# Kernel tuning notes

Hardware: AMD Instinct MI355X
Metric: run time of the kernel (lower is better)

The kernel has to match this reference:

```python
import jax, jax.numpy as jnp
import numpy as np

B, N, D = 512, 128, 768
TAU = 1.0            # NeuralSort temperature (allRank default)
COS_W = 0.1          # cosine_loss_weight
EPS = 1e-10          # allRank DEFAULT_EPS
PAD = -1.0           # allRank PADDED_Y_VALUE
SINKHORN_ITERS = 50
SINKHORN_TOL = 1e-6


def setup_inputs() -> dict:
    key = jax.random.key(0)
    kq, kr, ky = jax.random.split(key, 3)
    return {
        "query_embeddings": jax.random.normal(kq, (B, N, D), jnp.float32),
        "response_embeddings": jax.random.normal(kr, (B, N, D), jnp.float32),
        "labels": jax.random.uniform(ky, (B, N), dtype=jnp.float32),
    }


def _cosine_similarity(a, b):
    # torch.cosine_similarity semantics: clamp each norm at 1e-8
    num = jnp.sum(a * b, axis=-1)
    den = jnp.maximum(jnp.linalg.norm(a, axis=-1), 1e-8) * jnp.maximum(jnp.linalg.norm(b, axis=-1), 1e-8)
    return num / den


def _deterministic_neural_sort(s, tau, mask):
    # s: [B, N, 1] scores; mask: [B, N] padding mask (True = padded)
    n = s.shape[1]
    s = jnp.where(mask[:, :, None], -1e8, s)
    A = jnp.abs(s - jnp.swapaxes(s, 1, 2))                       # [B,N,N]
    pair_or = mask[:, :, None] | mask[:, None, :]
    A = jnp.where(pair_or, 0.0, A)
    Bmat = jnp.sum(A, axis=2, keepdims=True)                     # == A @ (1 1^T), broadcasts over cols
    valid = n - jnp.sum(mask, axis=1)                            # [B] number of non-padded items
    idx = jnp.arange(n)
    # per-row scaling vector: (n-m) - 1 - 2*j for j < n-m, else 0
    scaling = jnp.where(idx[None, :] < valid[:, None],
                        (valid[:, None] - 1 - 2 * idx[None, :]).astype(s.dtype), 0.0)
    s0 = jnp.where(mask[:, :, None], 0.0, s)
    C = s0 * scaling[:, None, :]                                 # [B,N,N] = s @ scaling^T
    P_max = jnp.swapaxes(C - Bmat, 1, 2)
    P_max = jnp.where(pair_or, -jnp.inf, P_max)
    P_max = jnp.where(mask[:, :, None] & mask[:, None, :], 1.0, P_max)
    return jax.nn.softmax(P_max / tau, axis=-1)


def _sinkhorn(mat, mask):
    pair_or = mask[:, None, :] | mask[:, :, None]
    pair_and = mask[:, None, :] & mask[:, :, None]
    mat = jnp.where(pair_or, 0.0, mat)
    mat = jnp.where(pair_and, 1.0, mat)

    def step(carry, _):
        m, done = carry
        m1 = m / jnp.maximum(jnp.sum(m, axis=1, keepdims=True), EPS)
        m2 = m1 / jnp.maximum(jnp.sum(m1, axis=2, keepdims=True), EPS)
        conv = (jnp.max(jnp.abs(jnp.sum(m2, axis=2) - 1.0)) < SINKHORN_TOL) & \
               (jnp.max(jnp.abs(jnp.sum(m2, axis=1) - 1.0)) < SINKHORN_TOL)
        new_m = jnp.where(done, m, m2)   # freeze once converged (emulates torch early break)
        return (new_m, done | conv), None

    (mat, _), _ = jax.lax.scan(step, (mat, jnp.array(False)), None, length=SINKHORN_ITERS)
    mat = jnp.where(pair_or, 0.0, mat)
    mat = jnp.where(pair_and, 1.0, mat)
    return mat


def _idcg_at_k(y_true, k):
    # allRank dcg(y_true, y_true, ats=[k]) with powered gains (no padding present)
    sorted_true = -jnp.sort(-y_true, axis=1)                     # descending
    gains = jnp.power(2.0, sorted_true) - 1.0
    discounts = 1.0 / jnp.log2(jnp.arange(y_true.shape[1], dtype=jnp.float32) + 2.0)
    return jnp.cumsum(gains * discounts, axis=1)[:, k - 1]       # [B]


def _forward(query_embeddings, response_embeddings, labels):
    scores = _cosine_similarity(query_embeddings, response_embeddings)   # [B,N]
    y_true = labels
    mask = (y_true == PAD)
    k = N                                                                # k=None -> slate length
    P_hat = _deterministic_neural_sort(scores[:, :, None], TAU, mask)    # [B,N,N]
    P_hat = _sinkhorn(P_hat, mask)
    P_hat = jnp.where(mask[:, :, None] | mask[:, None, :], 0.0, P_hat)
    g = jnp.power(2.0, jnp.where(mask, 0.0, y_true)) - 1.0               # powered relevancies
    ground_truth = jnp.einsum('bij,bj->bi', P_hat, g)                    # approx-sorted gains
    discounts = 1.0 / jnp.log2(jnp.arange(N, dtype=jnp.float32) + 2.0)
    discounted = ground_truth * discounts
    idcg = _idcg_at_k(y_true, k)                                         # [B]
    ndcg = jnp.sum(discounted[:, :k], axis=-1) / (idcg + EPS)
    idcg_zero = idcg == 0.0
    ndcg = jnp.where(idcg_zero, 0.0, ndcg)
    mean_ndcg = jnp.sum(ndcg) / jnp.maximum(jnp.sum(~idcg_zero), 1)
    ndcg_loss = 1.0 - mean_ndcg                                          # 1 + neuralNDCG = 1 - mean_ndcg
    cosine_loss = jnp.mean((scores - labels) ** 2)
    return (1.0 - COS_W) * ndcg_loss + COS_W * cosine_loss


def reference(query_embeddings, response_embeddings, labels):
    return _forward(query_embeddings, response_embeddings, labels)
```

## Files before the change

### kernel.cpp

```cpp
#include <hip/hip_runtime.h>
#include <math.h>

#define BB 512
#define NN 128
#define DD 768

__global__ __launch_bounds__(256, 2) void k_ndcg(const float* __restrict__ q,
                                                 const float* __restrict__ r,
                                                 const float* __restrict__ labels,
                                                 float* __restrict__ ndcg_out,
                                                 float* __restrict__ valid_out,
                                                 float* __restrict__ mse_out) {
    __shared__ float s_s[NN];
    __shared__ float s_B[NN];
    __shared__ float s_lab[NN];
    __shared__ float s_g[NN];
    __shared__ float s_u[NN];
    __shared__ float s_v[NN];
    __shared__ float s_rmax[NN];
    __shared__ float s_red[NN];
    __shared__ float s_mse[NN];
    __shared__ float s_gv[NN];
    __shared__ float s_wred[4];
    __shared__ float s_idcg[1];

    const int tid = threadIdx.x;
    const int b   = blockIdx.x;
    const int wv  = tid >> 6;
    const int ln  = tid & 63;
    const int p   = tid >> 1;
    const int h   = tid & 1;

    if (tid < NN) {
        float lv = labels[b * NN + tid];
        s_lab[tid] = lv;
        s_g[tid]   = exp2f(lv) - 1.0f;
    }

    const float4* q4 = (const float4*)(q + (size_t)b * NN * DD);
    const float4* r4 = (const float4*)(r + (size_t)b * NN * DD);
    for (int m = 0; m < 32; ++m) {
        const int row = wv + 4 * m;
        const float4* qa = q4 + row * (DD / 4);
        const float4* ra = r4 + row * (DD / 4);
        float qr = 0.f, qq = 0.f, rr2 = 0.f;
#pragma unroll
        for (int k = 0; k < 3; ++k) {
            float4 a = qa[ln + 64 * k];
            float4 c = ra[ln + 64 * k];
            qr  += a.x*c.x + a.y*c.y + a.z*c.z + a.w*c.w;
            qq  += a.x*a.x + a.y*a.y + a.z*a.z + a.w*a.w;
            rr2 += c.x*c.x + c.y*c.y + c.z*c.z + c.w*c.w;
        }
#pragma unroll
        for (int off = 32; off >= 1; off >>= 1) {
            qr  += __shfl_xor(qr, off);
            qq  += __shfl_xor(qq, off);
            rr2 += __shfl_xor(rr2, off);
        }
        if (ln == 0) {
            float den = fmaxf(sqrtf(qq), 1e-8f) * fmaxf(sqrtf(rr2), 1e-8f);
            s_s[row] = qr / den;
        }
    }
    __syncthreads();

    if (tid < NN) {
        float si = s_s[tid];
        float acc = 0.f;
        for (int j = 0; j < NN; ++j) acc += fabsf(si - s_s[j]);
        s_B[tid] = acc;
        float li = s_lab[tid];
        int rank = 0;
        for (int j = 0; j < NN; ++j) {
            float lj = s_lab[j];
            rank += (lj > li) || (lj == li && j < tid);
        }
        s_red[tid] = s_g[tid] / log2f((float)(rank + 2));
        float d = si - li;
        s_mse[tid] = d * d;
    }
    __syncthreads();
    if (tid < 32) {
        float v = s_red[tid] + s_red[tid + 32] + s_red[tid + 64] + s_red[tid + 96];
#pragma unroll
        for (int off = 16; off >= 1; off >>= 1) v += __shfl_xor(v, off);
        if (tid == 0) s_idcg[0] = v;
    } else if (tid < 64) {
        int t2 = tid - 32;
        float v = s_mse[t2] + s_mse[t2 + 32] + s_mse[t2 + 64] + s_mse[t2 + 96];
#pragma unroll
        for (int off = 16; off >= 1; off >>= 1) v = v + __shfl_xor(v, off);
        if (t2 == 0) mse_out[b] = v;
    }

    float u_p;
    float4 kr[16];
    {
        const float scal = (float)(127 - 2 * p);
        const float4* s4a = (const float4*)s_s;
        const float4* B4a = (const float4*)s_B;
        float rmax = -1e30f;
#pragma unroll
        for (int k = 0; k < 16; ++k) {
            float4 sv = s4a[16 * h + k];
            float4 Bv = B4a[16 * h + k];
            float4 v;
            v.x = sv.x * scal - Bv.x;
            v.y = sv.y * scal - Bv.y;
            v.z = sv.z * scal - Bv.z;
            v.w = sv.w * scal - Bv.w;
            kr[k] = v;
            rmax = fmaxf(rmax, fmaxf(fmaxf(v.x, v.y), fmaxf(v.z, v.w)));
        }
        rmax = fmaxf(rmax, __shfl_xor(rmax, 1));
        float rsum = 0.f;
#pragma unroll
        for (int k = 0; k < 16; ++k) {
            float4 v = kr[k];
            v.x = expf(v.x - rmax);
            v.y = expf(v.y - rmax);
            v.z = expf(v.z - rmax);
            v.w = expf(v.w - rmax);
            kr[k] = v;
            rsum += v.x + v.y + v.z + v.w;
        }
        rsum += __shfl_xor(rsum, 1);
        u_p = 1.0f / rsum;
        if (h == 0) { s_u[p] = u_p; s_rmax[p] = rmax; }
    }
    __syncthreads();

    float4 kc[16];
    {
        const float sp = s_s[p];
        const float Bp = s_B[p];
        const float4* rm4 = (const float4*)s_rmax;
#pragma unroll
        for (int k = 0; k < 16; ++k) {
            float4 rm = rm4[16 * h + k];
            const float base = (float)(127 - 2 * (64 * h + 4 * k));
            float4 e;
            e.x = expf(sp * base          - Bp - rm.x);
            e.y = expf(sp * (base - 2.f)  - Bp - rm.y);
            e.z = expf(sp * (base - 4.f)  - Bp - rm.z);
            e.w = expf(sp * (base - 6.f)  - Bp - rm.w);
            kc[k] = e;
        }
    }

    float v_p = 1.0f;
    const float4* u4 = (const float4*)s_u;
    const float4* v4 = (const float4*)s_v;
    for (int it = 0; it < 50; ++it) {
        float a = 0.f;
#pragma unroll
        for (int k = 0; k < 16; ++k) {
            float4 uu = u4[16 * h + k];
            float4 kk = kc[k];
            a += uu.x*kk.x + uu.y*kk.y + uu.z*kk.z + uu.w*kk.w;
        }
        a += __shfl_xor(a, 1);
        float cs  = v_p * a;
        float dev = fabsf(cs - 1.0f);
#pragma unroll
        for (int off = 2; off <= 32; off <<= 1) dev = fmaxf(dev, __shfl_xor(dev, off));
        if (ln == 0) s_wred[wv] = dev;
        __syncthreads();
        float devmax = fmaxf(fmaxf(s_wred[0], s_wred[1]), fmaxf(s_wred[2], s_wred[3]));
        if (it > 0 && devmax < 1e-6f) break;
        v_p = v_p / fmaxf(cs, 1e-10f);
        if (h == 0) s_v[p] = v_p;
        __syncthreads();
        float bb = 0.f;
#pragma unroll
        for (int k = 0; k < 16; ++k) {
            float4 vv = v4[16 * h + k];
            float4 kk = kr[k];
            bb += vv.x*kk.x + vv.y*kk.y + vv.z*kk.z + vv.w*kk.w;
        }
        bb += __shfl_xor(bb, 1);
        float rsm = u_p * bb;
        u_p = u_p / fmaxf(rsm, 1e-10f);
        if (h == 0) s_u[p] = u_p;
        __syncthreads();
    }

    if (tid < NN) s_gv[tid] = s_g[tid] * s_v[tid];
    __syncthreads();
    {
        const float4* gv4 = (const float4*)s_gv;
        float acc = 0.f;
#pragma unroll
        for (int k = 0; k < 16; ++k) {
            float4 gv = gv4[16 * h + k];
            float4 kk = kr[k];
            acc += kk.x*gv.x + kk.y*gv.y + kk.z*gv.z + kk.w*gv.w;
        }
        acc += __shfl_xor(acc, 1);
        if (h == 0) s_red[p] = u_p * acc / log2f((float)(p + 2));
    }
    __syncthreads();
    if (tid < 32) {
        float v = s_red[tid] + s_red[tid + 32] + s_red[tid + 64] + s_red[tid + 96];
#pragma unroll
        for (int off = 16; off >= 1; off >>= 1) v += __shfl_xor(v, off);
        if (tid == 0) {
            float idcg = s_idcg[0];
            bool zero = (idcg == 0.0f);
            ndcg_out[b]  = zero ? 0.0f : v / (idcg + 1e-10f);
            valid_out[b] = zero ? 0.0f : 1.0f;
        }
    }
}

__global__ __launch_bounds__(256) void k_final(const float* __restrict__ ndcg,
                                               const float* __restrict__ valid,
                                               const float* __restrict__ mse,
                                               float* __restrict__ out) {
    __shared__ float red[3][4];
    const int tid = threadIdx.x;
    const int lane = tid & 63, wv = tid >> 6;
    float nsum = ndcg[tid] + ndcg[tid + 256];
    float vsum = valid[tid] + valid[tid + 256];
    float msum = mse[tid] + mse[tid + 256];
#pragma unroll
    for (int off = 32; off >= 1; off >>= 1) {
        nsum += __shfl_xor(nsum, off);
        vsum += __shfl_xor(vsum, off);
        msum += __shfl_xor(msum, off);
    }
    if (lane == 0) { red[0][wv] = nsum; red[1][wv] = vsum; red[2][wv] = msum; }
    __syncthreads();
    if (tid == 0) {
        float n = red[0][0] + red[0][1] + red[0][2] + red[0][3];
        float v = red[1][0] + red[1][1] + red[1][2] + red[1][3];
        float m = red[2][0] + red[2][1] + red[2][2] + red[2][3];
        float mean_ndcg = n / fmaxf(v, 1.0f);
        out[0] = 0.9f * (1.0f - mean_ndcg) + 0.1f * (m / (float)(BB * NN));
    }
}

extern "C" void kernel_launch(void* const* d_in, const int* in_sizes, int n_in,
                              void* d_out, int out_size, void* d_ws, size_t ws_size,
                              hipStream_t stream) {
    const float* q   = (const float*)d_in[0];
    const float* r   = (const float*)d_in[1];
    const float* lab = (const float*)d_in[2];
    float* ndcg  = (float*)d_ws;
    float* valid = ndcg + BB;
    float* mse   = valid + BB;
    float* out   = (float*)d_out;

    k_ndcg<<<BB, 256, 0, stream>>>(q, r, lab, ndcg, valid, mse);
    k_final<<<1, 256, 0, stream>>>(ndcg, valid, mse, out);
}
```

Measured before the change: 451.3 us.

## Use 512 threads per slate with 4 lanes per row and fewer Sinkhorn barriers

Doubles the block to 512 threads so each Sinkhorn row is split across 4 lanes instead of 2. This halves the per-thread register arrays and the length of each dot product, and spreads the pairwise B/rank loop over all threads. The v-update is merged with the convergence-check barrier, removing one __syncthreads per iteration. Index rotation is added to spread LDS accesses across banks. The trade-off is more shuffle reductions and larger blocks, which may lower occupancy per CU.

```diff
diff --git a/kernel.cpp b/kernel.cpp
--- a/kernel.cpp
+++ b/kernel.cpp
@@ -5,7 +5,7 @@
 #define NN 128
 #define DD 768
 
-__global__ __launch_bounds__(256, 2) void k_ndcg(const float* __restrict__ q,
+__global__ __launch_bounds__(512, 4) void k_ndcg(const float* __restrict__ q,
                                                  const float* __restrict__ r,
                                                  const float* __restrict__ labels,
                                                  float* __restrict__ ndcg_out,
@@ -21,15 +21,15 @@
     __shared__ float s_red[NN];
     __shared__ float s_mse[NN];
     __shared__ float s_gv[NN];
-    __shared__ float s_wred[4];
+    __shared__ float s_wred[8];
     __shared__ float s_idcg[1];
 
     const int tid = threadIdx.x;
     const int b   = blockIdx.x;
     const int wv  = tid >> 6;
     const int ln  = tid & 63;
-    const int p   = tid >> 1;
-    const int h   = tid & 1;
+    const int p   = tid >> 2;
+    const int h   = tid & 3;
 
     if (tid < NN) {
         float lv = labels[b * NN + tid];
@@ -39,8 +39,8 @@
 
     const float4* q4 = (const float4*)(q + (size_t)b * NN * DD);
     const float4* r4 = (const float4*)(r + (size_t)b * NN * DD);
-    for (int m = 0; m < 32; ++m) {
-        const int row = wv + 4 * m;
+    for (int m = 0; m < 16; ++m) {
+        const int row = wv + 8 * m;
         const float4* qa = q4 + row * (DD / 4);
         const float4* ra = r4 + row * (DD / 4);
         float qr = 0.f, qq = 0.f, rr2 = 0.f;
@@ -65,20 +65,26 @@
     }
     __syncthreads();
 
-    if (tid < NN) {
-        float si = s_s[tid];
+    {
+        float si = s_s[p];
+        float li = s_lab[p];
         float acc = 0.f;
-        for (int j = 0; j < NN; ++j) acc += fabsf(si - s_s[j]);
-        s_B[tid] = acc;
-        float li = s_lab[tid];
         int rank = 0;
-        for (int j = 0; j < NN; ++j) {
+        for (int jj = 0; jj < 32; ++jj) {
+            int j = (h << 5) | ((jj + (h << 3)) & 31);
+            float sj = s_s[j];
             float lj = s_lab[j];
-            rank += (lj > li) || (lj == li && j < tid);
-        }
-        s_red[tid] = s_g[tid] / log2f((float)(rank + 2));
-        float d = si - li;
-        s_mse[tid] = d * d;
+            acc += fabsf(si - sj);
+            rank += (lj > li) || (lj == li && j < p);
+        }
+        acc  += __shfl_xor(acc, 1);  acc  += __shfl_xor(acc, 2);
+        rank += __shfl_xor(rank, 1); rank += __shfl_xor(rank, 2);
+        if (h == 0) {
+            s_B[p]   = acc;
+            s_red[p] = s_g[p] / log2f((float)(rank + 2));
+            float d  = si - li;
+            s_mse[p] = d * d;
+        }
     }
     __syncthreads();
     if (tid < 32) {
@@ -95,16 +101,16 @@
     }
 
     float u_p;
-    float4 kr[16];
+    float4 kr[8];
     {
         const float scal = (float)(127 - 2 * p);
         const float4* s4a = (const float4*)s_s;
         const float4* B4a = (const float4*)s_B;
         float rmax = -1e30f;
 #pragma unroll
-        for (int k = 0; k < 16; ++k) {
-            float4 sv = s4a[16 * h + k];
-            float4 Bv = B4a[16 * h + k];
+        for (int k = 0; k < 8; ++k) {
+            float4 sv = s4a[8 * h + k];
+            float4 Bv = B4a[8 * h + k];
             float4 v;
             v.x = sv.x * scal - Bv.x;
             v.y = sv.y * scal - Bv.y;
@@ -114,9 +120,10 @@
             rmax = fmaxf(rmax, fmaxf(fmaxf(v.x, v.y), fmaxf(v.z, v.w)));
         }
         rmax = fmaxf(rmax, __shfl_xor(rmax, 1));
+        rmax = fmaxf(rmax, __shfl_xor(rmax, 2));
         float rsum = 0.f;
 #pragma unroll
-        for (int k = 0; k < 16; ++k) {
+        for (int k = 0; k < 8; ++k) {
             float4 v = kr[k];
             v.x = expf(v.x - rmax);
             v.y = expf(v.y - rmax);
@@ -126,20 +133,21 @@
             rsum += v.x + v.y + v.z + v.w;
         }
         rsum += __shfl_xor(rsum, 1);
+        rsum += __shfl_xor(rsum, 2);
         u_p = 1.0f / rsum;
         if (h == 0) { s_u[p] = u_p; s_rmax[p] = rmax; }
     }
     __syncthreads();
 
-    float4 kc[16];
+    float4 kc[8];
     {
         const float sp = s_s[p];
         const float Bp = s_B[p];
         const float4* rm4 = (const float4*)s_rmax;
 #pragma unroll
-        for (int k = 0; k < 16; ++k) {
-            float4 rm = rm4[16 * h + k];
-            const float base = (float)(127 - 2 * (64 * h + 4 * k));
+        for (int k = 0; k < 8; ++k) {
+            float4 rm = rm4[8 * h + k];
+            const float base = (float)(127 - 2 * (32 * h + 4 * k));
             float4 e;
             e.x = expf(sp * base          - Bp - rm.x);
             e.y = expf(sp * (base - 2.f)  - Bp - rm.y);
@@ -152,52 +160,61 @@
     float v_p = 1.0f;
     const float4* u4 = (const float4*)s_u;
     const float4* v4 = (const float4*)s_v;
+    const float4* w4 = (const float4*)s_wred;
     for (int it = 0; it < 50; ++it) {
         float a = 0.f;
 #pragma unroll
-        for (int k = 0; k < 16; ++k) {
-            float4 uu = u4[16 * h + k];
-            float4 kk = kc[k];
-            a += uu.x*kk.x + uu.y*kk.y + uu.z*kk.z + uu.w*kk.w;
+        for (int k = 0; k < 8; ++k) {
+            int kk = (k + 2 * h) & 7;
+            float4 uu = u4[8 * h + kk];
+            float4 kv = kc[kk];
+            a += uu.x*kv.x + uu.y*kv.y + uu.z*kv.z + uu.w*kv.w;
         }
         a += __shfl_xor(a, 1);
-        float cs  = v_p * a;
-        float dev = fabsf(cs - 1.0f);
-#pragma unroll
-        for (int off = 2; off <= 32; off <<= 1) dev = fmaxf(dev, __shfl_xor(dev, off));
+        a += __shfl_xor(a, 2);
+        float cs    = v_p * a;
+        float v_new = v_p / fmaxf(cs, 1e-10f);
+        float dev   = fabsf(cs - 1.0f);
+#pragma unroll
+        for (int off = 4; off <= 32; off <<= 1) dev = fmaxf(dev, __shfl_xor(dev, off));
         if (ln == 0) s_wred[wv] = dev;
+        if (h == 0)  s_v[p] = v_new;
         __syncthreads();
-        float devmax = fmaxf(fmaxf(s_wred[0], s_wred[1]), fmaxf(s_wred[2], s_wred[3]));
+        float4 w0 = w4[0], w1 = w4[1];
+        float devmax = fmaxf(fmaxf(fmaxf(w0.x, w0.y), fmaxf(w0.z, w0.w)),
+                             fmaxf(fmaxf(w1.x, w1.y), fmaxf(w1.z, w1.w)));
         if (it > 0 && devmax < 1e-6f) break;
-        v_p = v_p / fmaxf(cs, 1e-10f);
-        if (h == 0) s_v[p] = v_p;
-        __syncthreads();
+        v_p = v_new;
         float bb = 0.f;
 #pragma unroll
-        for (int k = 0; k < 16; ++k) {
-            float4 vv = v4[16 * h + k];
-            float4 kk = kr[k];
-            bb += vv.x*kk.x + vv.y*kk.y + vv.z*kk.z + vv.w*kk.w;
+        for (int k = 0; k < 8; ++k) {
+            int kk = (k + 2 * h) & 7;
+            float4 vv = v4[8 * h + kk];
+            float4 kv = kr[kk];
+            bb += vv.x*kv.x + vv.y*kv.y + vv.z*kv.z + vv.w*kv.w;
         }
         bb += __shfl_xor(bb, 1);
+        bb += __shfl_xor(bb, 2);
         float rsm = u_p * bb;
         u_p = u_p / fmaxf(rsm, 1e-10f);
         if (h == 0) s_u[p] = u_p;
         __syncthreads();
     }
 
-    if (tid < NN) s_gv[tid] = s_g[tid] * s_v[tid];
+    if (h == 0) s_gv[p] = s_g[p] * v_p;
     __syncthreads();
     {
         const float4* gv4 = (const float4*)s_gv;
         float acc = 0.f;
 #pragma unroll
-        for (int k = 0; k < 16; ++k) {
-            float4 gv = gv4[16 * h + k];
-            float4 kk = kr[k];
-            acc += kk.x*gv.x + kk.y*gv.y + kk.z*gv.z + kk.w*gv.w;
+        for (int k = 0; k < 8; ++k) {
+            int kk = (k + 2 * h) & 7;
+            float4 gv = gv4[8 * h + kk];
+            float4 kv = kr[kk];
+            acc += kv.x*gv.x + kv.y*gv.y + kv.z*gv.z + kv.w*gv.w;
         }
         acc += __shfl_xor(acc, 1);
+        acc += __shfl_xor(acc, 2);
         if (h == 0) s_red[p] = u_p * acc / log2f((float)(p + 2));
     }
     __syncthreads();
@@ -252,6 +269,6 @@
     float* mse   = valid + BB;
     float* out   = (float*)d_out;
 
-    k_ndcg<<<BB, 256, 0, stream>>>(q, r, lab, ndcg, valid, mse);
+    k_ndcg<<<BB, 512, 0, stream>>>(q, r, lab, ndcg, valid, mse);
     k_final<<<1, 256, 0, stream>>>(ndcg, valid, mse, out);
 }
```

Measured after the change: 969.4 us. 2.15x slower.
